# Kernel tuning notes

Hardware: AMD Instinct MI355X
Metric: run time of the kernel (lower is better)

Reference implementation:

```python
import jax, jax.numpy as jnp
import numpy as np

N_OBJ, N_P, N2 = 16, 128, 2048
C, H, W = 256, 384, 384
IMG_W, IMG_H = 384.0, 384.0  # img_metas['img_shape'][:2][::-1]
SIM_THR = 0.0
LOSS_WEIGHT = 1.0
COS_EPS = 1e-8  # torch F.cosine_similarity default


def setup_inputs() -> dict:
    key = jax.random.key(0)
    k1, k2, k3, k4 = jax.random.split(key, 4)
    img_size = jnp.array([IMG_W, IMG_H], jnp.float32)
    point_set_1 = jax.random.uniform(k1, (N_OBJ, N_P, 2), jnp.float32) * img_size
    point_set_2 = jax.random.uniform(k2, (N_OBJ, N2, 2), jnp.float32) * img_size
    key_points = jax.random.uniform(k3, (N_OBJ * N_P, 2), jnp.float32) * img_size
    feats = jax.random.normal(k4, (1, C, H, W), jnp.float32)
    return {"point_set_1": point_set_1, "point_set_2": point_set_2,
            "feats": feats, "key_points": key_points}


def _grid_sample(img, pts01):
    # img: [C,H,W]; pts01: [P,2] (x,y) in [0,1]. Bilinear, align_corners=False,
    # zero padding -- matches mmcv point_sample / torch grid_sample.
    Ci, Hi, Wi = img.shape
    g = 2.0 * pts01 - 1.0
    x = ((g[:, 0] + 1.0) * Wi - 1.0) * 0.5
    y = ((g[:, 1] + 1.0) * Hi - 1.0) * 0.5
    x0 = jnp.floor(x)
    y0 = jnp.floor(y)
    wx1 = x - x0
    wy1 = y - y0

    def tap(xi, yi, wgt):
        valid = (xi >= 0) & (xi < Wi) & (yi >= 0) & (yi < Hi)
        xc = jnp.clip(xi, 0, Wi - 1).astype(jnp.int32)
        yc = jnp.clip(yi, 0, Hi - 1).astype(jnp.int32)
        return img[:, yc, xc] * (wgt * valid)[None, :]  # [C,P]

    return (tap(x0, y0, (1 - wx1) * (1 - wy1))
            + tap(x0 + 1, y0, wx1 * (1 - wy1))
            + tap(x0, y0 + 1, (1 - wx1) * wy1)
            + tap(x0 + 1, y0 + 1, wx1 * wy1))  # [C,P]


def reference(point_set_1, point_set_2, feats, key_points):
    img_size = jnp.array([IMG_W, IMG_H], feats.dtype)
    img = feats[0]  # feats.expand() reuses the same map for every object

    # feats_set_1: [n_obj, n_p, C]; feats_set_2: [n_obj, n2, C]
    f1 = _grid_sample(img, key_points / img_size).T.reshape(N_OBJ, N_P, C)
    f2 = _grid_sample(img, (point_set_2 / img_size).reshape(-1, 2)).T.reshape(N_OBJ, N2, C)

    # cosine similarity over channel dim (norms clamped to eps like torch)
    n1 = jnp.maximum(jnp.linalg.norm(f1, axis=-1), COS_EPS)  # [O,P]
    n2 = jnp.maximum(jnp.linalg.norm(f2, axis=-1), COS_EPS)  # [O,N2]
    sims = jnp.einsum('opc,onc->opn', f1, f2) / (n1[..., None] * n2[:, None, :])
    mask = sims >= SIM_THR  # [O,P,N2]

    # pairwise L2 distances between each key point and candidate set
    diff = point_set_1[:, :, None, :] - point_set_2[:, None, :, :]
    d = jnp.linalg.norm(diff, axis=-1)  # [O,P,N2]

    cnt = mask.sum(-1)  # [O,P]
    has = cnt > 0
    dmin = jnp.min(jnp.where(mask, d, jnp.inf), axis=-1)
    dmean = jnp.sum(jnp.where(mask, d, 0.0), axis=-1) / jnp.maximum(cnt, 1)
    # chamfer of a single point vs masked set: (nearest + mean)/2, 'mean' reduction
    m = (point_set_2.sum(axis=(1, 2)) >= 0).astype(d.dtype)  # [O]
    cost = jnp.where(has, 0.5 * (dmin + dmean), 0.0) * m[:, None]  # [O,P]

    dist = (cost.sum(-1) / N_P).mean()
    return dist * LOSS_WEIGHT
```

## Files before the change

### kernel.cpp

```cpp
#include <hip/hip_runtime.h>
#include <hip/hip_bf16.h>
#include <math.h>

#define W_    384
#define H_    384
#define HW_   (384*384)
#define C_    256
#define NOBJ  16
#define NP    128
#define N2    2048
#define NF1   (NOBJ*NP)
#define NPTS  (NOBJ*NP + NOBJ*N2)
#define NG    16
#define NT    8

typedef __attribute__((ext_vector_type(8))) short short8;
typedef __attribute__((ext_vector_type(4))) float f32x4;

__global__ __launch_bounds__(256) void k_transpose(const float* __restrict__ feats,
                                                   unsigned short* __restrict__ ftT) {
    __shared__ float tile[64][65];
    int b     = blockIdx.x;
    int pbase = (b % (HW_ / 64)) * 64;
    int cbase = (b / (HW_ / 64)) * 64;
    int lane  = threadIdx.x & 63;
    int grp   = threadIdx.x >> 6;

    #pragma unroll
    for (int r = 0; r < 16; ++r) {
        int c = r * 4 + grp;
        tile[c][lane] = feats[(size_t)(cbase + c) * HW_ + pbase + lane];
    }
    __syncthreads();
    #pragma unroll
    for (int r = 0; r < 16; ++r) {
        int p = r * 4 + grp;
        unsigned int u = __float_as_uint(tile[lane][p]);
        u += 0x7fffu + ((u >> 16) & 1u);
        ftT[(size_t)(pbase + p) * C_ + cbase + lane] = (unsigned short)(u >> 16);
    }
}

__global__ __launch_bounds__(256) void k_sample(const float* __restrict__ kpts,
                                                const float* __restrict__ ps2,
                                                const unsigned short* __restrict__ ftT,
                                                unsigned short* __restrict__ f12) {
    int point = blockIdx.x * 4 + (threadIdx.x >> 6);
    int lane  = threadIdx.x & 63;
    int cb    = lane * 4;

    const float* src = (point < NF1) ? (kpts + (size_t)point * 2)
                                     : (ps2 + (size_t)(point - NF1) * 2);
    float px = src[0], py = src[1];
    float x  = px - 0.5f;
    float y  = py - 0.5f;
    float x0 = floorf(x), y0 = floorf(y);
    int ix0 = (int)x0, iy0 = (int)y0;
    float fx = x - x0, fy = y - y0;

    float a0 = 0.f, a1 = 0.f, a2 = 0.f, a3 = 0.f;
    #pragma unroll
    for (int dy = 0; dy < 2; ++dy) {
        #pragma unroll
        for (int dx = 0; dx < 2; ++dx) {
            int ix = ix0 + dx, iy = iy0 + dy;
            float w = (dx ? fx : 1.f - fx) * (dy ? fy : 1.f - fy);
            if (ix >= 0 && ix < W_ && iy >= 0 && iy < H_) {
                const ushort4 t = *(const ushort4*)(ftT + ((size_t)(iy * W_ + ix) * C_ + cb));
                a0 += w * __uint_as_float((unsigned)t.x << 16);
                a1 += w * __uint_as_float((unsigned)t.y << 16);
                a2 += w * __uint_as_float((unsigned)t.z << 16);
                a3 += w * __uint_as_float((unsigned)t.w << 16);
            }
        }
    }
    ushort4 o;
    unsigned u;
    u = __float_as_uint(a0); u += 0x7fffu + ((u >> 16) & 1u); o.x = (unsigned short)(u >> 16);
    u = __float_as_uint(a1); u += 0x7fffu + ((u >> 16) & 1u); o.y = (unsigned short)(u >> 16);
    u = __float_as_uint(a2); u += 0x7fffu + ((u >> 16) & 1u); o.z = (unsigned short)(u >> 16);
    u = __float_as_uint(a3); u += 0x7fffu + ((u >> 16) & 1u); o.w = (unsigned short)(u >> 16);
    *(ushort4*)(f12 + (size_t)point * C_ + cb) = o;
}

__global__ __launch_bounds__(256) void k_sample_direct(const float* __restrict__ kpts,
                                                       const float* __restrict__ ps2,
                                                       const float* __restrict__ feats,
                                                       unsigned short* __restrict__ f12) {
    int point = blockIdx.x * 4 + (threadIdx.x >> 6);
    int lane  = threadIdx.x & 63;
    int cb    = lane * 4;

    const float* src = (point < NF1) ? (kpts + (size_t)point * 2)
                                     : (ps2 + (size_t)(point - NF1) * 2);
    float px = src[0], py = src[1];
    float x  = px - 0.5f, y = py - 0.5f;
    float x0 = floorf(x), y0 = floorf(y);
    int ix0 = (int)x0, iy0 = (int)y0;
    float fx = x - x0, fy = y - y0;

    float acc[4] = {0.f, 0.f, 0.f, 0.f};
    #pragma unroll
    for (int dy = 0; dy < 2; ++dy) {
        #pragma unroll
        for (int dx = 0; dx < 2; ++dx) {
            int ix = ix0 + dx, iy = iy0 + dy;
            float w = (dx ? fx : 1.f - fx) * (dy ? fy : 1.f - fy);
            if (ix >= 0 && ix < W_ && iy >= 0 && iy < H_) {
                int base = iy * W_ + ix;
                #pragma unroll
                for (int u = 0; u < 4; ++u)
                    acc[u] += w * feats[(size_t)(cb + u) * HW_ + base];
            }
        }
    }
    ushort4 o;
    unsigned u;
    u = __float_as_uint(acc[0]); u += 0x7fffu + ((u >> 16) & 1u); o.x = (unsigned short)(u >> 16);
    u = __float_as_uint(acc[1]); u += 0x7fffu + ((u >> 16) & 1u); o.y = (unsigned short)(u >> 16);
    u = __float_as_uint(acc[2]); u += 0x7fffu + ((u >> 16) & 1u); o.z = (unsigned short)(u >> 16);
    u = __float_as_uint(acc[3]); u += 0x7fffu + ((u >> 16) & 1u); o.w = (unsigned short)(u >> 16);
    *(ushort4*)(f12 + (size_t)point * C_ + cb) = o;
}

__global__ __launch_bounds__(256) void k_simdist(const unsigned short* __restrict__ f12,
                                                 const float* __restrict__ ps1,
                                                 const float* __restrict__ ps2,
                                                 float* __restrict__ pmin,
                                                 float* __restrict__ psum,
                                                 float* __restrict__ pcnt) {
    int wid  = blockIdx.x * 4 + (threadIdx.x >> 6);
    int lane = threadIdx.x & 63;
    int ng = wid & 15;
    int pt = (wid >> 4) & 7;
    int o  = wid >> 7;
    int quad = lane >> 4, col = lane & 15;

    const short* f12s = (const short*)f12;
    const short8* aptr =
        (const short8*)(f12s + ((size_t)(o * NP + pt * 16 + col) * C_ + quad * 8));
    short8 a[8];
    #pragma unroll
    for (int kb = 0; kb < 8; ++kb) a[kb] = aptr[kb * 4];

    const float2* ps1v = (const float2*)ps1;
    const float2* ps2v = (const float2*)ps2;
    float pxr[4], pyr[4];
    #pragma unroll
    for (int r = 0; r < 4; ++r) {
        float2 pc = ps1v[o * NP + pt * 16 + quad * 4 + r];
        pxr[r] = pc.x; pyr[r] = pc.y;
    }

    float mn[4] = {INFINITY, INFINITY, INFINITY, INFINITY};
    float sm[4] = {0.f, 0.f, 0.f, 0.f};
    float ct[4] = {0.f, 0.f, 0.f, 0.f};

    for (int t = 0; t < NT; ++t) {
        int nbase = ng * 128 + t * 16;
        const short8* bptr =
            (const short8*)(f12s + ((size_t)(NF1 + o * N2 + nbase + col) * C_ + quad * 8));
        f32x4 acc = {0.f, 0.f, 0.f, 0.f};
        #pragma unroll
        for (int kb = 0; kb < 8; ++kb)
            acc = __builtin_amdgcn_mfma_f32_16x16x32_bf16(a[kb], bptr[kb * 4], acc, 0, 0, 0);

        float2 nc = ps2v[o * N2 + nbase + col];
        #pragma unroll
        for (int r = 0; r < 4; ++r) {
            if (acc[r] >= 0.f) {
                float dx = pxr[r] - nc.x, dy = pyr[r] - nc.y;
                float d  = sqrtf(dx * dx + dy * dy);
                mn[r] = fminf(mn[r], d); sm[r] += d; ct[r] += 1.f;
            }
        }
    }

    #pragma unroll
    for (int r = 0; r < 4; ++r) {
        #pragma unroll
        for (int off = 1; off < 16; off <<= 1) {
            mn[r] = fminf(mn[r], __shfl_xor(mn[r], off, 16));
            sm[r] += __shfl_xor(sm[r], off, 16);
            ct[r] += __shfl_xor(ct[r], off, 16);
        }
    }
    if (col == 0) {
        #pragma unroll
        for (int r = 0; r < 4; ++r) {
            int p   = pt * 16 + quad * 4 + r;
            int idx = (o * NG + ng) * NP + p;
            pmin[idx] = mn[r]; psum[idx] = sm[r]; pcnt[idx] = ct[r];
        }
    }
}

__global__ __launch_bounds__(256) void k_final(const float* __restrict__ pmin,
                                               const float* __restrict__ psum,
                                               const float* __restrict__ pcnt,
                                               float* __restrict__ out) {
    int t = threadIdx.x;
    float tot = 0.f;
    for (int pair = t; pair < NOBJ * NP; pair += 256) {
        int o = pair >> 7, p = pair & 127;
        float mn = INFINITY, sm = 0.f, ct = 0.f;
        for (int g = 0; g < NG; ++g) {
            int idx = (o * NG + g) * NP + p;
            mn = fminf(mn, pmin[idx]);
            sm += psum[idx];
            ct += pcnt[idx];
        }
        if (ct > 0.f) tot += 0.5f * (mn + sm / ct);
    }
    #pragma unroll
    for (int off = 32; off; off >>= 1) tot += __shfl_xor(tot, off, 64);
    __shared__ float wsum[4];
    if ((t & 63) == 0) wsum[t >> 6] = tot;
    __syncthreads();
    if (t == 0)
        out[0] = (wsum[0] + wsum[1] + wsum[2] + wsum[3]) * (1.0f / (NOBJ * NP));
}

extern "C" void kernel_launch(void* const* d_in, const int* in_sizes, int n_in,
                              void* d_out, int out_size, void* d_ws, size_t ws_size,
                              hipStream_t stream) {
    const float* ps1   = (const float*)d_in[0];
    const float* ps2   = (const float*)d_in[1];
    const float* feats = (const float*)d_in[2];
    const float* kpts  = (const float*)d_in[3];
    float* out = (float*)d_out;

    const size_t sz_ftT  = (size_t)HW_ * C_ * sizeof(unsigned short);
    const size_t sz_f12  = (size_t)NPTS * C_ * sizeof(unsigned short);
    const size_t sz_part = (size_t)NOBJ * NG * NP * sizeof(float);

    char* ws = (char*)d_ws;
    if (ws_size >= sz_ftT + sz_f12 + 3 * sz_part) {
        unsigned short* ftT = (unsigned short*)ws;
        unsigned short* f12 = (unsigned short*)(ws + sz_ftT);
        float* pmin = (float*)(ws + sz_ftT + sz_f12);
        float* psum = (float*)(ws + sz_ftT + sz_f12 + sz_part);
        float* pcnt = (float*)(ws + sz_ftT + sz_f12 + 2 * sz_part);

        k_transpose<<<(HW_ / 64) * (C_ / 64), 256, 0, stream>>>(feats, ftT);
        k_sample<<<NPTS / 4, 256, 0, stream>>>(kpts, ps2, ftT, f12);
        k_simdist<<<NOBJ * 8 * NG / 4, 256, 0, stream>>>(f12, ps1, ps2, pmin, psum, pcnt);
        k_final<<<1, 256, 0, stream>>>(pmin, psum, pcnt, out);
    } else {
        unsigned short* f12 = (unsigned short*)ws;
        float* pmin = (float*)(ws + sz_f12);
        float* psum = (float*)(ws + sz_f12 + sz_part);
        float* pcnt = (float*)(ws + sz_f12 + 2 * sz_part);

        k_sample_direct<<<NPTS / 4, 256, 0, stream>>>(kpts, ps2, feats, f12);
        k_simdist<<<NOBJ * 8 * NG / 4, 256, 0, stream>>>(f12, ps1, ps2, pmin, psum, pcnt);
        k_final<<<1, 256, 0, stream>>>(pmin, psum, pcnt, out);
    }
}
```

Baseline: 277.7 us.

## Vectorize transpose, sampling, and partial-reduction memory accesses

Result: no change. 274.0 us (-1.3%).

```diff
diff --git a/kernel.cpp b/kernel.cpp
--- a/kernel.cpp
+++ b/kernel.cpp
@@ -17,27 +17,45 @@
 typedef __attribute__((ext_vector_type(8))) short short8;
 typedef __attribute__((ext_vector_type(4))) float f32x4;
 
+__device__ __forceinline__ unsigned short f2bf(float v) {
+    unsigned int u = __float_as_uint(v);
+    u += 0x7fffu + ((u >> 16) & 1u);
+    return (unsigned short)(u >> 16);
+}
+
 __global__ __launch_bounds__(256) void k_transpose(const float* __restrict__ feats,
                                                    unsigned short* __restrict__ ftT) {
     __shared__ float tile[64][65];
     int b     = blockIdx.x;
     int pbase = (b % (HW_ / 64)) * 64;
     int cbase = (b / (HW_ / 64)) * 64;
-    int lane  = threadIdx.x & 63;
-    int grp   = threadIdx.x >> 6;
-
-    #pragma unroll
-    for (int r = 0; r < 16; ++r) {
-        int c = r * 4 + grp;
-        tile[c][lane] = feats[(size_t)(cbase + c) * HW_ + pbase + lane];
+    int t     = threadIdx.x;
+
+    int p4 = (t & 15) * 4;
+    int c0 = t >> 4;
+    #pragma unroll
+    for (int pass = 0; pass < 4; ++pass) {
+        int c = c0 + pass * 16;
+        float4 v = *(const float4*)(feats + (size_t)(cbase + c) * HW_ + pbase + p4);
+        tile[c][p4 + 0] = v.x; tile[c][p4 + 1] = v.y;
+        tile[c][p4 + 2] = v.z; tile[c][p4 + 3] = v.w;
     }
     __syncthreads();
-    #pragma unroll
-    for (int r = 0; r < 16; ++r) {
-        int p = r * 4 + grp;
-        unsigned int u = __float_as_uint(tile[lane][p]);
-        u += 0x7fffu + ((u >> 16) & 1u);
-        ftT[(size_t)(pbase + p) * C_ + cbase + lane] = (unsigned short)(u >> 16);
+
+    int c8 = (t & 7) * 8;
+    int p0 = t >> 3;
+    #pragma unroll
+    for (int pass = 0; pass < 2; ++pass) {
+        int p = p0 + pass * 32;
+        unsigned short u[8];
+        #pragma unroll
+        for (int j = 0; j < 8; ++j) u[j] = f2bf(tile[c8 + j][p]);
+        uint4 pk;
+        pk.x = (unsigned)u[0] | ((unsigned)u[1] << 16);
+        pk.y = (unsigned)u[2] | ((unsigned)u[3] << 16);
+        pk.z = (unsigned)u[4] | ((unsigned)u[5] << 16);
+        pk.w = (unsigned)u[6] | ((unsigned)u[7] << 16);
+        *(uint4*)(ftT + (size_t)(pbase + p) * C_ + cbase + c8) = pk;
     }
 }
 
@@ -45,20 +63,22 @@
                                                 const float* __restrict__ ps2,
                                                 const unsigned short* __restrict__ ftT,
                                                 unsigned short* __restrict__ f12) {
-    int point = blockIdx.x * 4 + (threadIdx.x >> 6);
+    int wave  = blockIdx.x * 4 + (threadIdx.x >> 6);
     int lane  = threadIdx.x & 63;
-    int cb    = lane * 4;
+    int half  = lane >> 5;
+    int l32   = lane & 31;
+    int point = wave * 2 + half;
+    int cb    = l32 * 8;
 
     const float* src = (point < NF1) ? (kpts + (size_t)point * 2)
                                      : (ps2 + (size_t)(point - NF1) * 2);
-    float px = src[0], py = src[1];
-    float x  = px - 0.5f;
-    float y  = py - 0.5f;
+    float x  = src[0] - 0.5f;
+    float y  = src[1] - 0.5f;
     float x0 = floorf(x), y0 = floorf(y);
     int ix0 = (int)x0, iy0 = (int)y0;
     float fx = x - x0, fy = y - y0;
 
-    float a0 = 0.f, a1 = 0.f, a2 = 0.f, a3 = 0.f;
+    float a[8] = {0.f, 0.f, 0.f, 0.f, 0.f, 0.f, 0.f, 0.f};
     #pragma unroll
     for (int dy = 0; dy < 2; ++dy) {
         #pragma unroll
@@ -66,21 +86,24 @@
             int ix = ix0 + dx, iy = iy0 + dy;
             float w = (dx ? fx : 1.f - fx) * (dy ? fy : 1.f - fy);
             if (ix >= 0 && ix < W_ && iy >= 0 && iy < H_) {
-                const ushort4 t = *(const ushort4*)(ftT + ((size_t)(iy * W_ + ix) * C_ + cb));
-                a0 += w * __uint_as_float((unsigned)t.x << 16);
-                a1 += w * __uint_as_float((unsigned)t.y << 16);
-                a2 += w * __uint_as_float((unsigned)t.z << 16);
-                a3 += w * __uint_as_float((unsigned)t.w << 16);
+                uint4 tv = *(const uint4*)(ftT + ((size_t)(iy * W_ + ix) * C_ + cb));
+                a[0] += w * __uint_as_float(tv.x << 16);
+                a[1] += w * __uint_as_float(tv.x & 0xffff0000u);
+                a[2] += w * __uint_as_float(tv.y << 16);
+                a[3] += w * __uint_as_float(tv.y & 0xffff0000u);
+                a[4] += w * __uint_as_float(tv.z << 16);
+                a[5] += w * __uint_as_float(tv.z & 0xffff0000u);
+                a[6] += w * __uint_as_float(tv.w << 16);
+                a[7] += w * __uint_as_float(tv.w & 0xffff0000u);
             }
         }
     }
-    ushort4 o;
-    unsigned u;
-    u = __float_as_uint(a0); u += 0x7fffu + ((u >> 16) & 1u); o.x = (unsigned short)(u >> 16);
-    u = __float_as_uint(a1); u += 0x7fffu + ((u >> 16) & 1u); o.y = (unsigned short)(u >> 16);
-    u = __float_as_uint(a2); u += 0x7fffu + ((u >> 16) & 1u); o.z = (unsigned short)(u >> 16);
-    u = __float_as_uint(a3); u += 0x7fffu + ((u >> 16) & 1u); o.w = (unsigned short)(u >> 16);
-    *(ushort4*)(f12 + (size_t)point * C_ + cb) = o;
+    uint4 pk;
+    pk.x = (unsigned)f2bf(a[0]) | ((unsigned)f2bf(a[1]) << 16);
+    pk.y = (unsigned)f2bf(a[2]) | ((unsigned)f2bf(a[3]) << 16);
+    pk.z = (unsigned)f2bf(a[4]) | ((unsigned)f2bf(a[5]) << 16);
+    pk.w = (unsigned)f2bf(a[6]) | ((unsigned)f2bf(a[7]) << 16);
+    *(uint4*)(f12 + (size_t)point * C_ + cb) = pk;
 }
 
 __global__ __launch_bounds__(256) void k_sample_direct(const float* __restrict__ kpts,
@@ -93,8 +116,7 @@
 
     const float* src = (point < NF1) ? (kpts + (size_t)point * 2)
                                      : (ps2 + (size_t)(point - NF1) * 2);
-    float px = src[0], py = src[1];
-    float x  = px - 0.5f, y = py - 0.5f;
+    float x  = src[0] - 0.5f, y = src[1] - 0.5f;
     float x0 = floorf(x), y0 = floorf(y);
     int ix0 = (int)x0, iy0 = (int)y0;
     float fx = x - x0, fy = y - y0;
@@ -115,11 +137,7 @@
         }
     }
     ushort4 o;
-    unsigned u;
-    u = __float_as_uint(acc[0]); u += 0x7fffu + ((u >> 16) & 1u); o.x = (unsigned short)(u >> 16);
-    u = __float_as_uint(acc[1]); u += 0x7fffu + ((u >> 16) & 1u); o.y = (unsigned short)(u >> 16);
-    u = __float_as_uint(acc[2]); u += 0x7fffu + ((u >> 16) & 1u); o.z = (unsigned short)(u >> 16);
-    u = __float_as_uint(acc[3]); u += 0x7fffu + ((u >> 16) & 1u); o.w = (unsigned short)(u >> 16);
+    o.x = f2bf(acc[0]); o.y = f2bf(acc[1]); o.z = f2bf(acc[2]); o.w = f2bf(acc[3]);
     *(ushort4*)(f12 + (size_t)point * C_ + cb) = o;
 }
 
@@ -189,36 +207,44 @@
         #pragma unroll
         for (int r = 0; r < 4; ++r) {
             int p   = pt * 16 + quad * 4 + r;
-            int idx = (o * NG + ng) * NP + p;
+            int idx = (o * NP + p) * NG + ng;
             pmin[idx] = mn[r]; psum[idx] = sm[r]; pcnt[idx] = ct[r];
         }
     }
 }
 
-__global__ __launch_bounds__(256) void k_final(const float* __restrict__ pmin,
-                                               const float* __restrict__ psum,
-                                               const float* __restrict__ pcnt,
-                                               float* __restrict__ out) {
+__global__ __launch_bounds__(1024) void k_final(const float* __restrict__ pmin,
+                                                const float* __restrict__ psum,
+                                                const float* __restrict__ pcnt,
+                                                float* __restrict__ out) {
     int t = threadIdx.x;
     float tot = 0.f;
-    for (int pair = t; pair < NOBJ * NP; pair += 256) {
-        int o = pair >> 7, p = pair & 127;
+    for (int pair = t; pair < NOBJ * NP; pair += 1024) {
+        int base = pair * NG;
+        const float4* pm = (const float4*)(pmin + base);
+        const float4* ps = (const float4*)(psum + base);
+        const float4* pc = (const float4*)(pcnt + base);
         float mn = INFINITY, sm = 0.f, ct = 0.f;
-        for (int g = 0; g < NG; ++g) {
-            int idx = (o * NG + g) * NP + p;
-            mn = fminf(mn, pmin[idx]);
-            sm += psum[idx];
-            ct += pcnt[idx];
+        #pragma unroll
+        for (int g4 = 0; g4 < 4; ++g4) {
+            float4 a = pm[g4], b = ps[g4], c = pc[g4];
+            mn = fminf(mn, fminf(fminf(a.x, a.y), fminf(a.z, a.w)));
+            sm += b.x + b.y + b.z + b.w;
+            ct += c.x + c.y + c.z + c.w;
         }
         if (ct > 0.f) tot += 0.5f * (mn + sm / ct);
     }
     #pragma unroll
     for (int off = 32; off; off >>= 1) tot += __shfl_xor(tot, off, 64);
-    __shared__ float wsum[4];
+    __shared__ float wsum[16];
     if ((t & 63) == 0) wsum[t >> 6] = tot;
     __syncthreads();
-    if (t == 0)
-        out[0] = (wsum[0] + wsum[1] + wsum[2] + wsum[3]) * (1.0f / (NOBJ * NP));
+    if (t < 64) {
+        float v = (t < 16) ? wsum[t] : 0.f;
+        #pragma unroll
+        for (int off = 8; off; off >>= 1) v += __shfl_xor(v, off, 16);
+        if (t == 0) out[0] = v * (1.0f / (NOBJ * NP));
+    }
 }
 
 extern "C" void kernel_launch(void* const* d_in, const int* in_sizes, int n_in,
@@ -232,7 +258,7 @@
 
     const size_t sz_ftT  = (size_t)HW_ * C_ * sizeof(unsigned short);
     const size_t sz_f12  = (size_t)NPTS * C_ * sizeof(unsigned short);
-    const size_t sz_part = (size_t)NOBJ * NG * NP * sizeof(float);
+    const size_t sz_part = (size_t)NOBJ * NP * NG * sizeof(float);
 
     char* ws = (char*)d_ws;
     if (ws_size >= sz_ftT + sz_f12 + 3 * sz_part) {
@@ -243,9 +269,9 @@
         float* pcnt = (float*)(ws + sz_ftT + sz_f12 + 2 * sz_part);
 
         k_transpose<<<(HW_ / 64) * (C_ / 64), 256, 0, stream>>>(feats, ftT);
-        k_sample<<<NPTS / 4, 256, 0, stream>>>(kpts, ps2, ftT, f12);
+        k_sample<<<NPTS / 8, 256, 0, stream>>>(kpts, ps2, ftT, f12);
         k_simdist<<<NOBJ * 8 * NG / 4, 256, 0, stream>>>(f12, ps1, ps2, pmin, psum, pcnt);
-        k_final<<<1, 256, 0, stream>>>(pmin, psum, pcnt, out);
+        k_final<<<1, 1024, 0, stream>>>(pmin, psum, pcnt, out);
     } else {
         unsigned short* f12 = (unsigned short*)ws;
         float* pmin = (float*)(ws + sz_f12);
@@ -254,6 +280,6 @@
 
         k_sample_direct<<<NPTS / 4, 256, 0, stream>>>(kpts, ps2, feats, f12);
         k_simdist<<<NOBJ * 8 * NG / 4, 256, 0, stream>>>(f12, ps1, ps2, pmin, psum, pcnt);
-        k_final<<<1, 256, 0, stream>>>(pmin, psum, pcnt, out);
-    }
-}
+        k_final<<<1, 1024, 0, stream>>>(pmin, psum, pcnt, out);
+    }
+}
```
